# Optimization experiments

Hardware: AMD Instinct MI355X
Metric: run time of the kernel (lower is better)

## Reference

```python
import jax, jax.numpy as jnp
import numpy as np

NH, N = 48, 384
CARD, SUB, REPR, ENC = 16, 64, 1024, 1024
POOL_FEAT = 256 * 49


def _head_params(keys, app_size):
    k1, k2, k3 = keys
    W1 = jax.random.normal(k1, (CARD, app_size, SUB), jnp.float32) / np.sqrt(app_size)
    b1 = jnp.zeros((CARD, SUB), jnp.float32)
    W2 = jax.random.normal(k2, (CARD, REPR, SUB), jnp.float32) / np.sqrt(REPR)
    b2 = jnp.zeros((CARD, SUB), jnp.float32)
    W3 = jax.random.normal(k3, (CARD, SUB, REPR), jnp.float32) / np.sqrt(SUB)
    b3 = jnp.zeros((CARD, REPR), jnp.float32)
    return W1, b1, W2, b2, W3, b3


def setup_inputs() -> dict:
    key = jax.random.key(0)
    ks = list(jax.random.split(key, 24))
    d = {}
    d['box_features'] = jax.random.normal(ks[0], (N, POOL_FEAT), jnp.float32)
    d['feat3'] = jax.random.normal(ks[1], (1, 256, 25, 25), jnp.float32)
    d['spatial36'] = jax.random.uniform(ks[2], (NH * N, 36), jnp.float32)
    d['Wbh1'] = jax.random.normal(ks[3], (POOL_FEAT, ENC), jnp.float32) / np.sqrt(POOL_FEAT)
    d['bbh1'] = jnp.zeros(ENC, jnp.float32)
    d['Wbh2'] = jax.random.normal(ks[4], (ENC, ENC), jnp.float32) / np.sqrt(ENC)
    d['bbh2'] = jnp.zeros(ENC, jnp.float32)
    d['Wsp1'] = jax.random.normal(ks[5], (36, 128), jnp.float32) / 6.0
    d['bsp1'] = jnp.zeros(128, jnp.float32)
    d['Wsp2'] = jax.random.normal(ks[6], (128, 256), jnp.float32) / np.sqrt(128)
    d['bsp2'] = jnp.zeros(256, jnp.float32)
    d['Wsp3'] = jax.random.normal(ks[7], (256, REPR), jnp.float32) / 16.0
    d['bsp3'] = jnp.zeros(REPR, jnp.float32)
    d['Wadj'] = jax.random.normal(ks[8], (REPR, 1), jnp.float32) / 32.0
    d['badj'] = jnp.zeros(1, jnp.float32)
    for pre, app, k0 in (('A', 2 * ENC, 9), ('O', ENC, 12), ('S', ENC, 15), ('G', 256, 18)):
        W1, b1, W2, b2, W3, b3 = _head_params(ks[k0:k0 + 3], app)
        d[pre + '1W'], d[pre + '1b'] = W1, b1
        d[pre + '2W'], d[pre + '2b'] = W2, b2
        d[pre + '3W'], d[pre + '3b'] = W3, b3
    d['gln_h'] = jnp.ones(ENC, jnp.float32)
    d['bln_h'] = jnp.zeros(ENC, jnp.float32)
    d['gln_o'] = jnp.ones(ENC, jnp.float32)
    d['bln_o'] = jnp.zeros(ENC, jnp.float32)
    d['n_h'] = NH
    return d


def _attn_head(app, sp, W1, b1, W2, b2, W3, b3):
    # app [P_or_1, A], sp [P, REPR] -> relu(sum_c fc3_c(relu(fc1_c(app)*fc2_c(sp))))
    u = jnp.einsum('pa,cas->cps', app, W1) + b1[:, None, :]
    v = jnp.einsum('ps,csd->cpd', sp, W2) + b2[:, None, :]
    t = jax.nn.relu(u * v)  # broadcasts when app has leading 1
    return jax.nn.relu(jnp.einsum('cpd,cdr->pr', t, W3) + b3.sum(0))


def _msg_obj(app, sp, W1, b1, W2, b2, W3, b3):
    # app [n, ENC], sp [h, n, REPR] -> [h, n, REPR]  (object->subject messages)
    u = jnp.einsum('ne,ces->cns', app, W1) + b1[:, None, :]
    v = jnp.einsum('hns,csd->chnd', sp, W2) + b2[:, None, None, :]
    t = jax.nn.relu(u[:, None, :, :] * v)
    return jnp.einsum('chnd,cdr->hnr', t, W3) + b3.sum(0)


def _msg_hum(app, sp, W1, b1, W2, b2, W3, b3):
    # app [h, ENC], sp [h, n, REPR] -> [n, h, REPR]  (subject->object messages)
    u = jnp.einsum('he,ces->chs', app, W1) + b1[:, None, :]
    v = jnp.einsum('hns,csd->cnhd', sp, W2) + b2[:, None, None, :]
    t = jax.nn.relu(u[:, None, :, :] * v)
    return jnp.einsum('cnhd,cdr->nhr', t, W3) + b3.sum(0)


def _ln(x, g, b):
    mu = x.mean(-1, keepdims=True)
    var = jnp.mean((x - mu) ** 2, -1, keepdims=True)
    return (x - mu) * jax.lax.rsqrt(var + 1e-5) * g + b


def reference(box_features, feat3, spatial36, Wbh1, bbh1, Wbh2, bbh2,
              Wsp1, bsp1, Wsp2, bsp2, Wsp3, bsp3, Wadj, badj,
              A1W, A1b, A2W, A2b, A3W, A3b,
              O1W, O1b, O2W, O2b, O3W, O3b,
              S1W, S1b, S2W, S2b, S3W, S3b,
              G1W, G1b, G2W, G2b, G3W, G3b,
              gln_h, bln_h, gln_o, bln_o, n_h):
    h = int(n_h)
    n = box_features.shape[0]
    gfeat = feat3.mean(axis=(2, 3))  # [1, 256] (AdaptiveAvgPool2d(1) + flatten)
    # box_head MLP
    node = jax.nn.relu(box_features @ Wbh1 + bbh1)
    node = jax.nn.relu(node @ Wbh2 + bbh2)  # [n, ENC]
    # spatial_head MLP
    sp = jax.nn.relu(spatial36 @ Wsp1 + bsp1)
    sp = jax.nn.relu(sp @ Wsp2 + bsp2)
    sp = jax.nn.relu(sp @ Wsp3 + bsp3)  # [h*n, REPR]
    sp_r = sp.reshape(h, n, -1)
    x = np.repeat(np.arange(h), n)  # static pair indices
    y = np.tile(np.arange(n), h)
    h_node = node[:h]
    # one message-passing iteration (num_iter=1)
    pair_app = jnp.concatenate([h_node[x], node[y]], axis=1)  # [h*n, 2*ENC]
    w = _attn_head(pair_app, sp, A1W, A1b, A2W, A2b, A3W, A3b)
    adj = (w @ Wadj + badj).reshape(h, n)
    m_h = jax.nn.relu(jnp.sum(jax.nn.softmax(adj, axis=1)[..., None]
                              * _msg_obj(node, sp_r, O1W, O1b, O2W, O2b, O3W, O3b), axis=1))
    h_node = _ln(h_node + m_h, gln_h, bln_h)
    m_o = jax.nn.relu(jnp.sum(jax.nn.softmax(adj.T, axis=1)[..., None]
                              * _msg_hum(h_node, sp_r, S1W, S1b, S2W, S2b, S3W, S3b), axis=1))
    node = _ln(node + m_o, gln_o, bln_o)
    # static keep mask: drop pairs with identical indices (x != y)
    keep = x != y
    xk, yk = x[keep], y[keep]
    sp_k = sp_r[xk, yk]  # [Pk, REPR]
    f_pair = _attn_head(jnp.concatenate([h_node[xk], node[yk]], axis=1), sp_k,
                        A1W, A1b, A2W, A2b, A3W, A3b)
    f_glob = _attn_head(gfeat, sp_k, G1W, G1b, G2W, G2b, G3W, G3b)
    return jnp.concatenate([f_pair, f_glob], axis=1)  # [Pk, 2*REPR]
```

## Files before the change

kernel.cpp:

```cpp
#include <hip/hip_runtime.h>
#include <math.h>

#define NHH 48
#define NNN 384
#define NP  18432
#define NEC 1024

#define BM 128
#define BN 128
#define BK 32
#define KPAD 40

typedef __attribute__((ext_vector_type(8))) short short8v;
typedef __attribute__((ext_vector_type(4))) float f32x4;

__device__ __forceinline__ unsigned short f2bf(float x) {
  unsigned int u = __float_as_uint(x);
  u += 0x7fffu + ((u >> 16) & 1u);
  return (unsigned short)(u >> 16);
}
__device__ __forceinline__ float bf2f(unsigned short b) {
  return __uint_as_float(((unsigned)b) << 16);
}

__global__ __launch_bounds__(256) void convw_k(const float* __restrict__ in,
    unsigned short* __restrict__ out, int K, int N, int blocked)
{
  __shared__ float t[64][65];
  int kb = blockIdx.x * 64, nb = blockIdx.y * 64;
  const float* src; size_t stride;
  if (blocked) { src = in + (size_t)(nb >> 6) * K * 64; stride = 64; }
  else         { src = in + nb; stride = N; }
  for (int i = threadIdx.x; i < 64 * 64; i += 256) {
    int k = i >> 6, d = i & 63;
    t[d][k] = src[(size_t)(kb + k) * stride + d];
  }
  __syncthreads();
  for (int i = threadIdx.x; i < 64 * 64; i += 256) {
    int d = i >> 6, k = i & 63;
    out[(size_t)(nb + d) * K + kb + k] = f2bf(t[d][k]);
  }
}

__global__ __launch_bounds__(256) void cvt_k(const float* __restrict__ in,
    unsigned short* __restrict__ out, int n)
{
  int i = (blockIdx.x * 256 + threadIdx.x) * 4;
  if (i < n) {
    float4 v = *(const float4*)(in + i);
    uint2 o;
    o.x = (unsigned)f2bf(v.x) | ((unsigned)f2bf(v.y) << 16);
    o.y = (unsigned)f2bf(v.z) | ((unsigned)f2bf(v.w) << 16);
    *(uint2*)(out + i) = o;
  }
}

template<int MODE, int CBF16>
__global__ __launch_bounds__(256) void gemm_db(
    const unsigned short* __restrict__ A, const unsigned short* __restrict__ B,
    void* __restrict__ Cv, int M, int N, int K, int Ks,
    const float* __restrict__ bias, int do_relu,
    const float* __restrict__ x1, const float* __restrict__ x2,
    float* __restrict__ part, int colofs, int swz)
{
  __shared__ unsigned short As[2][BM * KPAD];
  __shared__ unsigned short Bs[2][BN * KPAD];
  __shared__ float red2[BM][2];

  const int tid  = threadIdx.x;
  const int lane = tid & 63;
  const int wave = tid >> 6;
  const int wr = wave >> 1, wc = wave & 1;
  const int lm = lane & 15;
  const int kg = lane >> 4;

  int bx = blockIdx.x, by = blockIdx.y;
  const int bz = blockIdx.z;
  if (swz) {
    int L = by * 8 + bx;
    int r = L & 7, q = L >> 3;
    bx = q & 7;
    by = r + ((q >> 3) << 3);
  }
  const int m0 = by * BM, n0 = bx * BN;
  const int kbeg = bz * Ks;
  const int kend = min(K, kbeg + Ks);
  const int nt = (kend - kbeg) / BK;

  f32x4 acc[4][4];
#pragma unroll
  for (int i = 0; i < 4; ++i)
#pragma unroll
    for (int j = 0; j < 4; ++j)
      acc[i][j] = (f32x4){0.f, 0.f, 0.f, 0.f};

  const int sr = tid >> 1;
  const int sc = (tid & 1) * 16;
  const unsigned short* aP = A + (size_t)(m0 + sr) * K + sc;
  const unsigned short* bP = B + (size_t)(n0 + sr) * K + sc;
  const int wofs = sr * KPAD + sc;

  uint4 ra0, ra1, rb0, rb1;
  uint4 sa0, sa1, sb0, sb1;

  auto fetchR = [&](int k0) {
    ra0 = *(const uint4*)(aP + k0); ra1 = *(const uint4*)(aP + k0 + 8);
    rb0 = *(const uint4*)(bP + k0); rb1 = *(const uint4*)(bP + k0 + 8);
  };
  auto fetchS = [&](int k0) {
    sa0 = *(const uint4*)(aP + k0); sa1 = *(const uint4*)(aP + k0 + 8);
    sb0 = *(const uint4*)(bP + k0); sb1 = *(const uint4*)(bP + k0 + 8);
  };
  auto writeR = [&](int buf) {
    *(uint4*)&As[buf][wofs] = ra0; *(uint4*)&As[buf][wofs + 8] = ra1;
    *(uint4*)&Bs[buf][wofs] = rb0; *(uint4*)&Bs[buf][wofs + 8] = rb1;
  };
  auto writeS = [&](int buf) {
    *(uint4*)&As[buf][wofs] = sa0; *(uint4*)&As[buf][wofs + 8] = sa1;
    *(uint4*)&Bs[buf][wofs] = sb0; *(uint4*)&Bs[buf][wofs + 8] = sb1;
  };
  auto computeBuf = [&](const unsigned short* as, const unsigned short* bs) {
    const int lk = kg * 8;
    short8v af[4], bfr[4];
#pragma unroll
    for (int mi = 0; mi < 4; ++mi)
      af[mi] = *(const short8v*)&as[(wr * 64 + mi * 16 + lm) * KPAD + lk];
#pragma unroll
    for (int nj = 0; nj < 4; ++nj)
      bfr[nj] = *(const short8v*)&bs[(wc * 64 + nj * 16 + lm) * KPAD + lk];
#pragma unroll
    for (int mi = 0; mi < 4; ++mi)
#pragma unroll
      for (int nj = 0; nj < 4; ++nj)
        acc[mi][nj] = __builtin_amdgcn_mfma_f32_16x16x32_bf16(af[mi], bfr[nj], acc[mi][nj], 0, 0, 0);
  };

  fetchR(kbeg);
  if (nt > 1) fetchS(kbeg + BK);
  writeR(0);
  if (nt > 2) fetchR(kbeg + 2 * BK);
  __syncthreads();

  for (int it = 0; it < nt; it += 2) {
    writeS(1);
    if (it + 3 < nt) fetchS(kbeg + (it + 3) * BK);
    computeBuf(&As[0][0], &Bs[0][0]);
    __syncthreads();
    if (it + 2 < nt) writeR(0);
    if (it + 4 < nt) fetchR(kbeg + (it + 4) * BK);
    computeBuf(&As[1][0], &Bs[1][0]);
    __syncthreads();
  }

  const int rbase = m0 + wr * 64;
  const int cbase = n0 + wc * 64;

  if constexpr (MODE == 0 || MODE == 3) {
#pragma unroll
    for (int mi = 0; mi < 4; ++mi)
#pragma unroll
      for (int r = 0; r < 4; ++r) {
        int grow = rbase + mi * 16 + kg * 4 + r;
#pragma unroll
        for (int nj = 0; nj < 4; ++nj) {
          int gcol = cbase + nj * 16 + lm;
          float t = acc[mi][nj][r] + (bias ? bias[gcol] : 0.f);
          float v;
          if constexpr (MODE == 3) v = fmaxf(x1[gcol] * t, 0.f);
          else                     v = do_relu ? fmaxf(t, 0.f) : t;
          size_t idx = (size_t)grow * N + gcol;
          if constexpr (CBF16) ((unsigned short*)Cv)[idx] = f2bf(v);
          else                 ((float*)Cv)[idx] = v;
        }
      }
  } else if constexpr (MODE == 5) {
    size_t zofs = (size_t)bz * M;
#pragma unroll
    for (int mi = 0; mi < 4; ++mi)
#pragma unroll
      for (int r = 0; r < 4; ++r) {
        int grow = rbase + mi * 16 + kg * 4 + r;
#pragma unroll
        for (int nj = 0; nj < 4; ++nj) {
          int gcol = cbase + nj * 16 + lm;
          part[(zofs + grow) * N + gcol] = acc[mi][nj][r];
        }
      }
  } else if constexpr (MODE == 2) {
#pragma unroll
    for (int mi = 0; mi < 4; ++mi)
#pragma unroll
      for (int r = 0; r < 4; ++r) {
        int grow = rbase + mi * 16 + kg * 4 + r;
        int h = grow / NNN, n = grow - h * NNN;
        if (n == h) continue;
        long long orow = grow - h - (n > h ? 1 : 0);
#pragma unroll
        for (int nj = 0; nj < 4; ++nj) {
          int gcol = cbase + nj * 16 + lm;
          float v = fmaxf(acc[mi][nj][r] + bias[gcol], 0.f);
          ((float*)Cv)[orow * 2048 + colofs + gcol] = v;
        }
      }
  } else if constexpr (MODE == 1) {
#pragma unroll
    for (int mi = 0; mi < 4; ++mi)
#pragma unroll
      for (int r = 0; r < 4; ++r) {
        float s = 0.f;
#pragma unroll
        for (int nj = 0; nj < 4; ++nj) {
          int gcol = cbase + nj * 16 + lm;
          float v = fmaxf(acc[mi][nj][r] + bias[gcol], 0.f);
          s = fmaf(v, x1[gcol], s);
        }
#pragma unroll
        for (int off2 = 1; off2 < 16; off2 <<= 1) s += __shfl_xor(s, off2);
        if (lm == 0) red2[wr * 64 + mi * 16 + kg * 4 + r][wc] = s;
      }
    __syncthreads();
    if (tid < BM) {
      part[(size_t)(m0 + tid) * 8 + bx] = red2[tid][0] + red2[tid][1];
    }
  }
}

__global__ __launch_bounds__(256) void tmulb_k(const unsigned short* __restrict__ vA,
    const float* __restrict__ uh, const float* __restrict__ un,
    unsigned short* __restrict__ V)
{
  int p = blockIdx.x;
  int h = p / NNN, n = p - h * NNN;
  int j = threadIdx.x * 4;
  const float* uhr = uh + (size_t)h * NEC + j;
  const float* unr = un + (size_t)n * NEC + j;
  uint2 w = *(const uint2*)(vA + (size_t)p * NEC + j);
  float v0 = bf2f((unsigned short)(w.x & 0xffff));
  float v1 = bf2f((unsigned short)(w.x >> 16));
  float v2 = bf2f((unsigned short)(w.y & 0xffff));
  float v3 = bf2f((unsigned short)(w.y >> 16));
  float f0 = fmaxf((uhr[0] + unr[0]) * v0, 0.f);
  float f1 = fmaxf((uhr[1] + unr[1]) * v1, 0.f);
  float f2 = fmaxf((uhr[2] + unr[2]) * v2, 0.f);
  float f3 = fmaxf((uhr[3] + unr[3]) * v3, 0.f);
  uint2 o;
  o.x = (unsigned)f2bf(f0) | ((unsigned)f2bf(f1) << 16);
  o.y = (unsigned)f2bf(f2) | ((unsigned)f2bf(f3) << 16);
  *(uint2*)(V + (size_t)p * NEC + j) = o;
}

template<int MODE, int ABF16, int BBF16, int CBF16>
__global__ __launch_bounds__(256) void gemm_mfma(
    const void* __restrict__ Av, const void* __restrict__ Bv, long long ldbBlock,
    void* __restrict__ Cv, int M, int N, int K, int Ks,
    const float* __restrict__ bias, int do_relu,
    const float* __restrict__ x1, const float* __restrict__ x2,
    float* __restrict__ part, int colofs, int swz)
{
  __shared__ unsigned short As[BM * KPAD];
  __shared__ unsigned short Bs[BN * KPAD];

  const float* Af = (const float*)Av;
  const unsigned short* Ab = (const unsigned short*)Av;
  const float* Bf = (const float*)Bv;
  const unsigned short* Bb = (const unsigned short*)Bv;

  const int tid  = threadIdx.x;
  const int lane = tid & 63;
  const int wave = tid >> 6;
  const int wr = wave >> 1, wc = wave & 1;
  const int lm = lane & 15;
  const int kg = lane >> 4;

  int bx = blockIdx.x, by = blockIdx.y, bz = blockIdx.z;
  if (swz == 2) {
    int gy = gridDim.y;
    int ntile = gy * gridDim.z;
    int L = (bz * gy + by) * 8 + bx;
    int r = L & 7, q = L >> 3;
    int tpx = ntile >> 3;
    int tile = r * tpx + (q >> 3);
    bx = q & 7;
    bz = tile / gy;
    by = tile - bz * gy;
  }
  const int m0 = by * BM, n0 = bx * BN;
  const int kbeg = bz * Ks;
  const int kend = min(K, kbeg + Ks);

  f32x4 acc[4][4];
#pragma unroll
  for (int i = 0; i < 4; ++i)
#pragma unroll
    for (int j = 0; j < 4; ++j)
      acc[i][j] = (f32x4){0.f, 0.f, 0.f, 0.f};

  const int bn = tid & 127;
  const int kb = (tid >> 7) * 16;
  const float* bsrc = nullptr; long long bstride = 0;
  if constexpr (!BBF16) {
    int gcol = n0 + bn;
    if (ldbBlock) { bsrc = Bf + (long long)(gcol >> 6) * ldbBlock + (gcol & 63); bstride = 64; }
    else          { bsrc = Bf + gcol; bstride = N; }
  }

  uint4 pa0 = {0,0,0,0}, pa1 = {0,0,0,0};
  uint2 qa0 = {0,0}, qa1 = {0,0}, qa2 = {0,0}, qa3 = {0,0};
  uint4 pb0 = {0,0,0,0}, pb1 = {0,0,0,0};

  auto fetchA = [&](int k0) {
    if constexpr (ABF16) {
      int m = tid >> 1, kh = (tid & 1) * 16;
      int gm = m0 + m;
      pa0 = (uint4){0,0,0,0}; pa1 = (uint4){0,0,0,0};
      if (gm < M) {
        const uint4* s = (const uint4*)(Ab + (size_t)gm * K + k0 + kh);
        pa0 = s[0]; pa1 = s[1];
      }
    } else {
#define LOADA_F32(J, DST) { \
      int m = (tid >> 3) + J * 32; int k = (tid & 7) * 4; \
      int gm = m0 + m, gk = k0 + k; \
      float x0=0.f, x1v=0.f, x2v=0.f, x3=0.f; \
      if (gm < M) { const float* src = Af + (long long)gm * K + gk; \
        if (gk + 3 < K) { float4 v = *(const float4*)src; x0=v.x; x1v=v.y; x2v=v.z; x3=v.w; } \
        else { if (gk < K) x0 = src[0]; if (gk+1 < K) x1v = src[1]; \
               if (gk+2 < K) x2v = src[2]; if (gk+3 < K) x3 = src[3]; } } \
      DST.x = (unsigned)f2bf(x0)  | ((unsigned)f2bf(x1v) << 16); \
      DST.y = (unsigned)f2bf(x2v) | ((unsigned)f2bf(x3)  << 16); }
      LOADA_F32(0, qa0) LOADA_F32(1, qa1) LOADA_F32(2, qa2) LOADA_F32(3, qa3)
#undef LOADA_F32
    }
  };
  auto fetchB = [&](int k0) {
    if constexpr (BBF16) {
      int nrow = tid >> 1, kh = (tid & 1) * 16;
      const uint4* s = (const uint4*)(Bb + (size_t)(n0 + nrow) * K + k0 + kh);
      pb0 = s[0]; pb1 = s[1];
    } else {
#define PACKB(I, DST) { int g0 = k0 + kb + 2*I, g1 = g0 + 1; \
      float a = (g0 < K) ? bsrc[(long long)g0 * bstride] : 0.f; \
      float c = (g1 < K) ? bsrc[(long long)g1 * bstride] : 0.f; \
      DST = (unsigned)f2bf(a) | ((unsigned)f2bf(c) << 16); }
      PACKB(0, pb0.x) PACKB(1, pb0.y) PACKB(2, pb0.z) PACKB(3, pb0.w)
      PACKB(4, pb1.x) PACKB(5, pb1.y) PACKB(6, pb1.z) PACKB(7, pb1.w)
#undef PACKB
    }
  };
  auto stage = [&]() {
    if constexpr (ABF16) {
      int m = tid >> 1, kh = (tid & 1) * 16;
      *(uint4*)&As[m * KPAD + kh]     = pa0;
      *(uint4*)&As[m * KPAD + kh + 8] = pa1;
    } else {
      int m = tid >> 3, k = (tid & 7) * 4;
      *(uint2*)&As[(m      ) * KPAD + k] = qa0;
      *(uint2*)&As[(m +  32) * KPAD + k] = qa1;
      *(uint2*)&As[(m +  64) * KPAD + k] = qa2;
      *(uint2*)&As[(m +  96) * KPAD + k] = qa3;
    }
    if constexpr (BBF16) {
      int nrow = tid >> 1, kh = (tid & 1) * 16;
      *(uint4*)&Bs[nrow * KPAD + kh]     = pb0;
      *(uint4*)&Bs[nrow * KPAD + kh + 8] = pb1;
    } else {
      *(uint4*)&Bs[bn * KPAD + kb]     = pb0;
      *(uint4*)&Bs[bn * KPAD + kb + 8] = pb1;
    }
  };

  fetchA(kbeg); fetchB(kbeg);
  for (int k0 = kbeg; k0 < kend; k0 += BK) {
    stage();
    int kn = k0 + BK;
    if (kn < kend) { fetchA(kn); fetchB(kn); }
    __syncthreads();
    {
      const int lk = kg * 8;
      short8v af[4], bfr[4];
#pragma unroll
      for (int mi = 0; mi < 4; ++mi)
        af[mi] = *(const short8v*)&As[(wr * 64 + mi * 16 + lm) * KPAD + lk];
#pragma unroll
      for (int nj = 0; nj < 4; ++nj)
        bfr[nj] = *(const short8v*)&Bs[(wc * 64 + nj * 16 + lm) * KPAD + lk];
#pragma unroll
      for (int mi = 0; mi < 4; ++mi)
#pragma unroll
        for (int nj = 0; nj < 4; ++nj)
          acc[mi][nj] = __builtin_amdgcn_mfma_f32_16x16x32_bf16(af[mi], bfr[nj], acc[mi][nj], 0, 0, 0);
    }
    __syncthreads();
  }

  const int rbase = m0 + wr * 64;
  const int cbase = n0 + wc * 64;

  if constexpr (MODE == 0) {
#pragma unroll
    for (int mi = 0; mi < 4; ++mi)
#pragma unroll
      for (int r = 0; r < 4; ++r) {
        int grow = rbase + mi * 16 + kg * 4 + r;
        if (grow >= M) continue;
#pragma unroll
        for (int nj = 0; nj < 4; ++nj) {
          int gcol = cbase + nj * 16 + lm;
          float t = acc[mi][nj][r] + (bias ? bias[gcol] : 0.f);
          float v = do_relu ? fmaxf(t, 0.f) : t;
          size_t idx = (size_t)grow * N + gcol;
          if constexpr (CBF16) ((unsigned short*)Cv)[idx] = f2bf(v);
          else                 ((float*)Cv)[idx] = v;
        }
      }
  } else if constexpr (MODE == 5) {
    size_t zofs = (size_t)bz * M;
#pragma unroll
    for (int mi = 0; mi < 4; ++mi)
#pragma unroll
      for (int r = 0; r < 4; ++r) {
        int grow = rbase + mi * 16 + kg * 4 + r;
        if (grow >= M) continue;
#pragma unroll
        for (int nj = 0; nj < 4; ++nj) {
          int gcol = cbase + nj * 16 + lm;
          part[(zofs + grow) * N + gcol] = acc[mi][nj][r];
        }
      }
  }
}

__global__ __launch_bounds__(256) void ksum_k(const float* __restrict__ P,
    const float* __restrict__ bias, int do_relu, float* __restrict__ C,
    int MN, int N, int S)
{
  int i = blockIdx.x * 256 + threadIdx.x;
  if (i < MN) {
    float s = 0.f;
    for (int z = 0; z < S; ++z) s += P[(size_t)z * MN + i];
    if (bias) s += bias[i % N];
    C[i] = do_relu ? fmaxf(s, 0.f) : s;
  }
}

__global__ __launch_bounds__(256) void tw_k(const unsigned short* __restrict__ V,
    const float* __restrict__ uO, const float* __restrict__ soft, float* __restrict__ tw)
{
  int h = blockIdx.x;
  int j = blockIdx.y * 256 + threadIdx.x;
  const float* srow = soft + h * NNN;
  float s = 0.f;
  for (int n = 0; n < NNN; ++n) {
    float v = bf2f(V[((size_t)h * NNN + n) * NEC + j]);
    float t = fmaxf(uO[(size_t)n * NEC + j] * v, 0.f);
    s = fmaf(srow[n], t, s);
  }
  tw[(size_t)h * NEC + j] = s;
}

__global__ __launch_bounds__(256) void two_k(const unsigned short* __restrict__ V,
    const float* __restrict__ uS, const float* __restrict__ softT, float* __restrict__ two)
{
  int n = blockIdx.x;
  int j = blockIdx.y * 256 + threadIdx.x;
  const float* srow = softT + n * NHH;
  float s = 0.f;
#pragma unroll 8
  for (int h = 0; h < NHH; ++h) {
    float v = bf2f(V[((size_t)h * NNN + n) * NEC + j]);
    float t = fmaxf(uS[(size_t)h * NEC + j] * v, 0.f);
    s = fmaf(srow[h], t, s);
  }
  two[(size_t)n * NEC + j] = s;
}

__global__ void adjfin_k(const float* __restrict__ part, const float* __restrict__ badj,
                         float* __restrict__ adj)
{
  int p = blockIdx.x * blockDim.x + threadIdx.x;
  if (p < NP) {
    float s = badj[0];
#pragma unroll
    for (int c = 0; c < 8; ++c) s += part[(size_t)p * 8 + c];
    adj[p] = s;
  }
}

__global__ __launch_bounds__(64) void softmax_row_k(const float* __restrict__ adj,
                                                    float* __restrict__ soft)
{
  __shared__ float buf[NNN];
  int h = blockIdx.x, t = threadIdx.x;
  float mx = -1e30f;
  for (int n = t; n < NNN; n += 64) { float v = adj[h * NNN + n]; buf[n] = v; mx = fmaxf(mx, v); }
#pragma unroll
  for (int off = 32; off >= 1; off >>= 1) mx = fmaxf(mx, __shfl_xor(mx, off));
  float s = 0.f;
  for (int n = t; n < NNN; n += 64) { float e = expf(buf[n] - mx); buf[n] = e; s += e; }
#pragma unroll
  for (int off = 32; off >= 1; off >>= 1) s += __shfl_xor(s, off);
  float inv = 1.f / s;
  for (int n = t; n < NNN; n += 64) soft[h * NNN + n] = buf[n] * inv;
}

__global__ __launch_bounds__(64) void softmaxT_k(const float* __restrict__ adj,
                                                 float* __restrict__ softT)
{
  int n = blockIdx.x, t = threadIdx.x;
  float v = (t < NHH) ? adj[t * NNN + n] : -1e30f;
  float mx = v;
#pragma unroll
  for (int off = 32; off >= 1; off >>= 1) mx = fmaxf(mx, __shfl_xor(mx, off));
  float e = (t < NHH) ? expf(v - mx) : 0.f;
  float s = e;
#pragma unroll
  for (int off = 32; off >= 1; off >>= 1) s += __shfl_xor(s, off);
  if (t < NHH) softT[n * NHH + t] = e / s;
}

__global__ __launch_bounds__(256) void ln_k(const float* __restrict__ x, const float* __restrict__ m,
    const float* __restrict__ g, const float* __restrict__ b, float* __restrict__ out)
{
  int r = blockIdx.x, t = threadIdx.x;
  __shared__ float rs[4], rs2[4];
  const float* xr = x + (size_t)r * NEC;
  const float* mr = m + (size_t)r * NEC;
  float s = 0.f, s2 = 0.f;
  for (int j = t; j < NEC; j += 256) { float v = xr[j] + mr[j]; s += v; s2 = fmaf(v, v, s2); }
#pragma unroll
  for (int off = 32; off >= 1; off >>= 1) { s += __shfl_xor(s, off); s2 += __shfl_xor(s2, off); }
  if ((t & 63) == 0) { rs[t >> 6] = s; rs2[t >> 6] = s2; }
  __syncthreads();
  s = rs[0] + rs[1] + rs[2] + rs[3];
  s2 = rs2[0] + rs2[1] + rs2[2] + rs2[3];
  float mean = s * (1.f / NEC);
  float var = s2 * (1.f / NEC) - mean * mean;
  float rstd = rsqrtf(var + 1e-5f);
  float* o = out + (size_t)r * NEC;
  for (int j = t; j < NEC; j += 256) {
    float v = xr[j] + mr[j];
    o[j] = (v - mean) * rstd * g[j] + b[j];
  }
}

__global__ __launch_bounds__(64) void gfeat_k(const float* __restrict__ feat3,
                                              float* __restrict__ gfeat)
{
  int ch = blockIdx.x, t = threadIdx.x;
  float s = 0.f;
  for (int i = t; i < 625; i += 64) s += feat3[ch * 625 + i];
#pragma unroll
  for (int off = 32; off >= 1; off >>= 1) s += __shfl_xor(s, off);
  if (t == 0) gfeat[ch] = s * (1.f / 625.f);
}

__global__ __launch_bounds__(256) void b3sum_k(const float* __restrict__ b3,
                                               float* __restrict__ out)
{
  int r = blockIdx.x * 256 + threadIdx.x;
  if (r < NEC) {
    float s = 0.f;
#pragma unroll
    for (int c = 0; c < 16; ++c) s += b3[c * NEC + r];
    out[r] = s;
  }
}

extern "C" void kernel_launch(void* const* d_in, const int* in_sizes, int n_in,
                              void* d_out, int out_size, void* d_ws, size_t ws_size,
                              hipStream_t stream)
{
  const float* box   = (const float*)d_in[0];
  const float* feat3 = (const float*)d_in[1];
  const float* sp36  = (const float*)d_in[2];
  const float* Wbh1  = (const float*)d_in[3];
  const float* bbh1  = (const float*)d_in[4];
  const float* Wbh2  = (const float*)d_in[5];
  const float* bbh2  = (const float*)d_in[6];
  const float* Wsp1  = (const float*)d_in[7];
  const float* bsp1  = (const float*)d_in[8];
  const float* Wsp2  = (const float*)d_in[9];
  const float* bsp2  = (const float*)d_in[10];
  const float* Wsp3  = (const float*)d_in[11];
  const float* bsp3  = (const float*)d_in[12];
  const float* Wadj  = (const float*)d_in[13];
  const float* badj  = (const float*)d_in[14];
  const float* A1W = (const float*)d_in[15]; const float* A1b = (const float*)d_in[16];
  const float* A2W = (const float*)d_in[17]; const float* A2b = (const float*)d_in[18];
  const float* A3W = (const float*)d_in[19]; const float* A3b = (const float*)d_in[20];
  const float* O1W = (const float*)d_in[21]; const float* O1b = (const float*)d_in[22];
  const float* O2W = (const float*)d_in[23]; const float* O2b = (const float*)d_in[24];
  const float* O3W = (const float*)d_in[25]; const float* O3b = (const float*)d_in[26];
  const float* S1W = (const float*)d_in[27]; const float* S1b = (const float*)d_in[28];
  const float* S2W = (const float*)d_in[29]; const float* S2b = (const float*)d_in[30];
  const float* S3W = (const float*)d_in[31]; const float* S3b = (const float*)d_in[32];
  const float* G1W = (const float*)d_in[33]; const float* G1b = (const float*)d_in[34];
  const float* G2W = (const float*)d_in[35]; const float* G2b = (const float*)d_in[36];
  const float* G3W = (const float*)d_in[37]; const float* G3b = (const float*)d_in[38];
  const float* gln_h = (const float*)d_in[39]; const float* bln_h = (const float*)d_in[40];
  const float* gln_o = (const float*)d_in[41]; const float* bln_o = (const float*)d_in[42];
  (void)in_sizes; (void)n_in; (void)out_size; (void)ws_size;

  char* base = (char*)d_ws;
  unsigned short* Vb  = (unsigned short*)base;
  float* partial      = (float*)base;
  unsigned short* s1  = Vb;
  unsigned short* s2  = Vb + (size_t)NP * 128;
  unsigned short* SPb = (unsigned short*)(base + (size_t)NP * NEC * 2);
  float* f = (float*)(base + (size_t)NP * NEC * 4);
  size_t off = 0;
  auto alloc = [&](size_t n) { float* p = f + off; off += n; return p; };
  float* node1 = alloc(384 * NEC);
  float* node  = alloc(384 * NEC);
  float* hnode1= alloc(48 * NEC);
  float* node2 = alloc(384 * NEC);
  float* uhA   = alloc(48 * NEC);
  float* unA   = alloc(384 * NEC);
  float* uO    = alloc(384 * NEC);
  float* uS    = alloc(48 * NEC);
  float* uh2   = alloc(48 * NEC);
  float* un2   = alloc(384 * NEC);
  float* uG    = alloc(NEC);
  float* gfeat = alloc(256);
  float* b3A = alloc(NEC); float* b3O = alloc(NEC); float* b3S = alloc(NEC); float* b3G = alloc(NEC);
  float* part  = alloc((size_t)NP * 8);
  float* adj   = alloc(NP);
  float* soft  = alloc(NP);
  float* softT = alloc(NP);
  float* twb   = alloc(48 * NEC);
  float* twob  = alloc(384 * NEC);
  float* m_h   = alloc(48 * NEC);
  float* m_o   = alloc(384 * NEC);
  unsigned short* wb = (unsigned short*)(f + off);
  size_t wo = 0;
  auto walloc = [&](size_t n) { unsigned short* p = wb + wo; wo += n; return p; };
  unsigned short* A2Wb  = walloc((size_t)NEC * NEC);
  unsigned short* O2Wb  = walloc((size_t)NEC * NEC);
  unsigned short* S2Wb  = walloc((size_t)NEC * NEC);
  unsigned short* G2Wb  = walloc((size_t)NEC * NEC);
  unsigned short* A3Wb  = walloc((size_t)NEC * NEC);
  unsigned short* G3Wb  = walloc((size_t)NEC * NEC);
  unsigned short* Wsp3b = walloc((size_t)NEC * 256);
  unsigned short* Wsp2b = walloc((size_t)256 * 128);
  unsigned short* vAb   = walloc((size_t)NP * NEC);
  unsigned short* Wbh1b = walloc((size_t)NEC * 12544);
  unsigned short* boxb  = walloc((size_t)384 * 12544);

  auto gS = [&](const float* A, const float* B, long long lb, float* C,
                int M, int N, int K, const float* bias, int relu, int S) {
    int Ks = ((K + S * BK - 1) / (S * BK)) * BK;
    dim3 grid(N / BN, (M + BM - 1) / BM, S);
    hipLaunchKernelGGL((gemm_mfma<5, 0, 0, 0>), grid, dim3(256), 0, stream,
                       A, B, lb, nullptr, M, N, K, Ks, nullptr, 0,
                       nullptr, nullptr, partial, 0, 2);
    int MN = M * N;
    hipLaunchKernelGGL(ksum_k, dim3((MN + 255) / 256), dim3(256), 0, stream,
                       partial, bias, relu, C, MN, N, S);
  };
  auto convw = [&](const float* W, unsigned short* Wb2, int K, int N, int blocked) {
    dim3 g(K / 64, N / 64);
    hipLaunchKernelGGL(convw_k, g, dim3(256), 0, stream, W, Wb2, K, N, blocked);
  };

  convw(A2W, A2Wb, NEC, NEC, 1);
  convw(O2W, O2Wb, NEC, NEC, 1);
  convw(S2W, S2Wb, NEC, NEC, 1);
  convw(G2W, G2Wb, NEC, NEC, 1);
  convw(A3W, A3Wb, NEC, NEC, 0);
  convw(G3W, G3Wb, NEC, NEC, 0);
  convw(Wsp3, Wsp3b, 256, NEC, 0);
  convw(Wsp2, Wsp2b, 128, 256, 0);
  convw(Wbh1, Wbh1b, 12544, NEC, 0);
  cvt_k<<<(384 * 12544 / 4 + 255) / 256, 256, 0, stream>>>(box, boxb, 384 * 12544);

  gfeat_k<<<256, 64, 0, stream>>>(feat3, gfeat);
  b3sum_k<<<4, 256, 0, stream>>>(A3b, b3A);
  b3sum_k<<<4, 256, 0, stream>>>(O3b, b3O);
  b3sum_k<<<4, 256, 0, stream>>>(S3b, b3S);
  b3sum_k<<<4, 256, 0, stream>>>(G3b, b3G);

  {
    dim3 grid(NEC / BN, 384 / BM, 28);
    hipLaunchKernelGGL((gemm_db<5, 0>), grid, dim3(256), 0, stream,
                       boxb, Wbh1b, nullptr, 384, NEC, 12544, 448, nullptr, 0,
                       nullptr, nullptr, partial, 0, 0);
    int MN = 384 * NEC;
    hipLaunchKernelGGL(ksum_k, dim3((MN + 255) / 256), dim3(256), 0, stream,
                       partial, bbh1, 1, node1, MN, NEC, 28);
  }
  gS(node1, Wbh2, 0, node, 384, NEC, NEC, bbh2, 1, 16);

  dim3 gBig(8, NP / BM);

  {
    dim3 g1(1, NP / BM); dim3 g2(2, NP / BM);
    hipLaunchKernelGGL((gemm_mfma<0, 0, 0, 1>), g1, dim3(256), 0, stream,
                       sp36, Wsp1, 0LL, s1, NP, 128, 36, 36, bsp1, 1, nullptr, nullptr, nullptr, 0, 0);
    hipLaunchKernelGGL((gemm_db<0, 1>), g2, dim3(256), 0, stream,
                       s1, Wsp2b, s2, NP, 256, 128, 128, bsp2, 1, nullptr, nullptr, nullptr, 0, 0);
    hipLaunchKernelGGL((gemm_db<0, 1>), gBig, dim3(256), 0, stream,
                       s2, Wsp3b, SPb, NP, NEC, 256, 256, bsp3, 1, nullptr, nullptr, nullptr, 0, 1);
  }

  hipLaunchKernelGGL((gemm_db<0, 1>), gBig, dim3(256), 0, stream,
                     SPb, A2Wb, vAb, NP, NEC, NEC, NEC, A2b, 0, nullptr, nullptr, nullptr, 0, 1);

  gS(node, A1W,             2048LL * 64, uhA, 48,  NEC, NEC, A1b,    0, 16);
  gS(node, A1W + 1024 * 64, 2048LL * 64, unA, 384, NEC, NEC, nullptr, 0, 16);
  tmulb_k<<<NP, 256, 0, stream>>>(vAb, uhA, unA, Vb);
  hipLaunchKernelGGL((gemm_db<1, 0>), gBig, dim3(256), 0, stream,
                     Vb, A3Wb, nullptr, NP, NEC, NEC, NEC, b3A, 1, Wadj, nullptr, part, 0, 1);
  adjfin_k<<<(NP + 255) / 256, 256, 0, stream>>>(part, badj, adj);
  softmax_row_k<<<NHH, 64, 0, stream>>>(adj, soft);
  softmaxT_k<<<NNN, 64, 0, stream>>>(adj, softT);

  gS(node, O1W, 1024LL * 64, uO, 384, NEC, NEC, O1b, 0, 16);
  hipLaunchKernelGGL((gemm_db<0, 1>), gBig, dim3(256), 0, stream,
                     SPb, O2Wb, Vb, NP, NEC, NEC, NEC, O2b, 0, nullptr, nullptr, nullptr, 0, 1);
  tw_k<<<dim3(NHH, 4), 256, 0, stream>>>(Vb, uO, soft, twb);
  gS(twb, O3W, 0, m_h, 48, NEC, NEC, b3O, 1, 16);
  ln_k<<<NHH, 256, 0, stream>>>(node, m_h, gln_h, bln_h, hnode1);

  gS(hnode1, S1W, 1024LL * 64, uS, 48, NEC, NEC, S1b, 0, 16);
  hipLaunchKernelGGL((gemm_db<0, 1>), gBig, dim3(256), 0, stream,
                     SPb, S2Wb, Vb, NP, NEC, NEC, NEC, S2b, 0, nullptr, nullptr, nullptr, 0, 1);
  two_k<<<dim3(NNN, 4), 256, 0, stream>>>(Vb, uS, softT, twob);
  gS(twob, S3W, 0, m_o, 384, NEC, NEC, b3S, 1, 16);
  ln_k<<<NNN, 256, 0, stream>>>(node, m_o, gln_o, bln_o, node2);

  gS(hnode1, A1W,             2048LL * 64, uh2, 48,  NEC, NEC, A1b,    0, 16);
  gS(node2,  A1W + 1024 * 64, 2048LL * 64, un2, 384, NEC, NEC, nullptr, 0, 16);
  tmulb_k<<<NP, 256, 0, stream>>>(vAb, uh2, un2, Vb);
  hipLaunchKernelGGL((gemm_db<2, 0>), gBig, dim3(256), 0, stream,
                     Vb, A3Wb, (float*)d_out, NP, NEC, NEC, NEC, b3A, 1, nullptr, nullptr, nullptr, 0, 1);

  {
    dim3 g1(8, 1);
    hipLaunchKernelGGL((gemm_mfma<0, 0, 0, 0>), g1, dim3(256), 0, stream,
                       gfeat, G1W, 256LL * 64, uG, 1, NEC, 256, 256, G1b, 0, nullptr, nullptr, nullptr, 0, 0);
  }
  hipLaunchKernelGGL((gemm_db<3, 1>), gBig, dim3(256), 0, stream,
                     SPb, G2Wb, Vb, NP, NEC, NEC, NEC, G2b, 0, uG, nullptr, nullptr, 0, 1);
  hipLaunchKernelGGL((gemm_db<2, 0>), gBig, dim3(256), 0, stream,
                     Vb, G3Wb, (float*)d_out, NP, NEC, NEC, NEC, b3G, 1, nullptr, nullptr, nullptr, 1024, 1);
}
```

Measured before the change: 870.5 us.

## Batch the four spatial fc2 GEMMs into one wide GEMM and group node projections

The four separate SP×W2 GEMMs (A, O, S, G heads) become one NP×4096 GEMM that reads SP once. Its epilogue applies the per-column bias and, for the G slice, the uG gating. The small node-side projections (uhA/unA/uO, uS/uh2) are grouped into wider bf16 split-K GEMMs with a grouped reduction kernel, and the fp32 mfma GEMMs are replaced with bf16 gemm_db. This removes repeated reads of SP and several launches. The cost is a larger workspace holding the 4096-wide V buffer and strided accesses in the downstream consumers.

```diff
diff --git a/kernel.cpp b/kernel.cpp
--- a/kernel.cpp
+++ b/kernel.cpp
@@ -5,6 +5,7 @@
 #define NNN 384
 #define NP  18432
 #define NEC 1024
+#define MB1 (1024*1024)
 
 #define BM 128
 #define BN 128
@@ -24,21 +25,21 @@
 }
 
 __global__ __launch_bounds__(256) void convw_k(const float* __restrict__ in,
-    unsigned short* __restrict__ out, int K, int N, int blocked)
+    unsigned short* __restrict__ out, int inK, int outK, int N, int blocked, int koff)
 {
   __shared__ float t[64][65];
   int kb = blockIdx.x * 64, nb = blockIdx.y * 64;
   const float* src; size_t stride;
-  if (blocked) { src = in + (size_t)(nb >> 6) * K * 64; stride = 64; }
+  if (blocked) { src = in + (size_t)(nb >> 6) * inK * 64; stride = 64; }
   else         { src = in + nb; stride = N; }
   for (int i = threadIdx.x; i < 64 * 64; i += 256) {
     int k = i >> 6, d = i & 63;
-    t[d][k] = src[(size_t)(kb + k) * stride + d];
+    t[d][k] = src[(size_t)(kb + koff + k) * stride + d];
   }
   __syncthreads();
   for (int i = threadIdx.x; i < 64 * 64; i += 256) {
     int d = i >> 6, k = i & 63;
-    out[(size_t)(nb + d) * K + kb + k] = f2bf(t[d][k]);
+    out[(size_t)(nb + d) * outK + kb + k] = f2bf(t[d][k]);
   }
 }
 
@@ -55,9 +56,22 @@
   }
 }
 
+__global__ __launch_bounds__(256) void biascat4_k(const float* __restrict__ b0,
+    const float* __restrict__ b1, const float* __restrict__ b2,
+    const float* __restrict__ b3, float* __restrict__ out)
+{
+  int j = blockIdx.x * 256 + threadIdx.x;
+  if (j < 4096) {
+    int g = j >> 10, c = j & 1023;
+    const float* b = g == 0 ? b0 : (g == 1 ? b1 : (g == 2 ? b2 : b3));
+    out[j] = b[c];
+  }
+}
+
 template<int MODE, int CBF16>
 __global__ __launch_bounds__(256) void gemm_db(
-    const unsigned short* __restrict__ A, const unsigned short* __restrict__ B,
+    const unsigned short* __restrict__ A, int lda,
+    const unsigned short* __restrict__ B, int ldb,
     void* __restrict__ Cv, int M, int N, int K, int Ks,
     const float* __restrict__ bias, int do_relu,
     const float* __restrict__ x1, const float* __restrict__ x2,
@@ -77,10 +91,11 @@
   int bx = blockIdx.x, by = blockIdx.y;
   const int bz = blockIdx.z;
   if (swz) {
-    int L = by * 8 + bx;
+    int gx = gridDim.x;
+    int L = by * gx + bx;
     int r = L & 7, q = L >> 3;
-    bx = q & 7;
-    by = r + ((q >> 3) << 3);
+    bx = q % gx;
+    by = r + 8 * (q / gx);
   }
   const int m0 = by * BM, n0 = bx * BN;
   const int kbeg = bz * Ks;
@@ -96,8 +111,8 @@
 
   const int sr = tid >> 1;
   const int sc = (tid & 1) * 16;
-  const unsigned short* aP = A + (size_t)(m0 + sr) * K + sc;
-  const unsigned short* bP = B + (size_t)(n0 + sr) * K + sc;
+  const unsigned short* aP = A + (size_t)(m0 + sr) * lda + sc;
+  const unsigned short* bP = B + (size_t)(n0 + sr) * ldb + sc;
   const int wofs = sr * KPAD + sc;
 
   uint4 ra0, ra1, rb0, rb1;
@@ -155,7 +170,7 @@
   const int rbase = m0 + wr * 64;
   const int cbase = n0 + wc * 64;
 
-  if constexpr (MODE == 0 || MODE == 3) {
+  if constexpr (MODE == 0) {
 #pragma unroll
     for (int mi = 0; mi < 4; ++mi)
 #pragma unroll
@@ -165,12 +180,24 @@
         for (int nj = 0; nj < 4; ++nj) {
           int gcol = cbase + nj * 16 + lm;
           float t = acc[mi][nj][r] + (bias ? bias[gcol] : 0.f);
-          float v;
-          if constexpr (MODE == 3) v = fmaxf(x1[gcol] * t, 0.f);
-          else                     v = do_relu ? fmaxf(t, 0.f) : t;
+          float v = do_relu ? fmaxf(t, 0.f) : t;
           size_t idx = (size_t)grow * N + gcol;
           if constexpr (CBF16) ((unsigned short*)Cv)[idx] = f2bf(v);
           else                 ((float*)Cv)[idx] = v;
+        }
+      }
+  } else if constexpr (MODE == 6) {
+#pragma unroll
+    for (int mi = 0; mi < 4; ++mi)
+#pragma unroll
+      for (int r = 0; r < 4; ++r) {
+        int grow = rbase + mi * 16 + kg * 4 + r;
+#pragma unroll
+        for (int nj = 0; nj < 4; ++nj) {
+          int gcol = cbase + nj * 16 + lm;
+          float t = acc[mi][nj][r] + bias[gcol];
+          float v = (gcol >= 3072) ? fmaxf(x1[gcol - 3072] * t, 0.f) : t;
+          ((unsigned short*)Cv)[(size_t)grow * N + gcol] = f2bf(v);
         }
       }
   } else if constexpr (MODE == 5) {
@@ -226,7 +253,7 @@
 }
 
 __global__ __launch_bounds__(256) void tmulb_k(const unsigned short* __restrict__ vA,
-    const float* __restrict__ uh, const float* __restrict__ un,
+    int vstride, const float* __restrict__ uh, const float* __restrict__ un,
     unsigned short* __restrict__ V)
 {
   int p = blockIdx.x;
@@ -234,7 +261,7 @@
   int j = threadIdx.x * 4;
   const float* uhr = uh + (size_t)h * NEC + j;
   const float* unr = un + (size_t)n * NEC + j;
-  uint2 w = *(const uint2*)(vA + (size_t)p * NEC + j);
+  uint2 w = *(const uint2*)(vA + (size_t)p * vstride + j);
   float v0 = bf2f((unsigned short)(w.x & 0xffff));
   float v1 = bf2f((unsigned short)(w.x >> 16));
   float v2 = bf2f((unsigned short)(w.y & 0xffff));
@@ -443,7 +470,27 @@
   }
 }
 
-__global__ __launch_bounds__(256) void tw_k(const unsigned short* __restrict__ V,
+__global__ __launch_bounds__(256) void ksumg_k(const float* __restrict__ P,
+    const float* __restrict__ b0, const float* __restrict__ b1, const float* __restrict__ b2,
+    float* __restrict__ C0, float* __restrict__ C1, float* __restrict__ C2,
+    int M, int NG, int S)
+{
+  int i = blockIdx.x * 256 + threadIdx.x;
+  int N = NG << 10;
+  int total = M * N;
+  if (i < total) {
+    int m = i / N, c = i - m * N;
+    int g = c >> 10, col = c & 1023;
+    float s = 0.f;
+    for (int z = 0; z < S; ++z) s += P[(size_t)z * total + i];
+    const float* b = g == 0 ? b0 : (g == 1 ? b1 : b2);
+    if (b) s += b[col];
+    float* C = g == 0 ? C0 : (g == 1 ? C1 : C2);
+    C[(size_t)m * 1024 + col] = s;
+  }
+}
+
+__global__ __launch_bounds__(256) void tw_k(const unsigned short* __restrict__ V, int sV,
     const float* __restrict__ uO, const float* __restrict__ soft, float* __restrict__ tw)
 {
   int h = blockIdx.x;
@@ -451,14 +498,14 @@
   const float* srow = soft + h * NNN;
   float s = 0.f;
   for (int n = 0; n < NNN; ++n) {
-    float v = bf2f(V[((size_t)h * NNN + n) * NEC + j]);
+    float v = bf2f(V[((size_t)h * NNN + n) * sV + j]);
     float t = fmaxf(uO[(size_t)n * NEC + j] * v, 0.f);
     s = fmaf(srow[n], t, s);
   }
   tw[(size_t)h * NEC + j] = s;
 }
 
-__global__ __launch_bounds__(256) void two_k(const unsigned short* __restrict__ V,
+__global__ __launch_bounds__(256) void two_k(const unsigned short* __restrict__ V, int sV,
     const float* __restrict__ uS, const float* __restrict__ softT, float* __restrict__ two)
 {
   int n = blockIdx.x;
@@ -467,7 +514,7 @@
   float s = 0.f;
 #pragma unroll 8
   for (int h = 0; h < NHH; ++h) {
-    float v = bf2f(V[((size_t)h * NNN + n) * NEC + j]);
+    float v = bf2f(V[((size_t)h * NNN + n) * sV + j]);
     float t = fmaxf(uS[(size_t)h * NEC + j] * v, 0.f);
     s = fmaf(srow[h], t, s);
   }
@@ -602,27 +649,30 @@
   (void)in_sizes; (void)n_in; (void)out_size; (void)ws_size;
 
   char* base = (char*)d_ws;
-  unsigned short* Vb  = (unsigned short*)base;
-  float* partial      = (float*)base;
+  unsigned short* V4  = (unsigned short*)base;
+  float* partialV4    = (float*)base;
+  unsigned short* Vb  = (unsigned short*)(base + (size_t)NP * 4096 * 2);
+  float* partialVb    = (float*)Vb;
   unsigned short* s1  = Vb;
   unsigned short* s2  = Vb + (size_t)NP * 128;
-  unsigned short* SPb = (unsigned short*)(base + (size_t)NP * NEC * 2);
-  float* f = (float*)(base + (size_t)NP * NEC * 4);
+  unsigned short* SPb = Vb + (size_t)NP * 1024;
+  float* f = (float*)(SPb + (size_t)NP * 1024);
   size_t off = 0;
   auto alloc = [&](size_t n) { float* p = f + off; off += n; return p; };
   float* node1 = alloc(384 * NEC);
   float* node  = alloc(384 * NEC);
-  float* hnode1= alloc(48 * NEC);
+  float* hnode1= alloc(128 * NEC);
   float* node2 = alloc(384 * NEC);
-  float* uhA   = alloc(48 * NEC);
+  float* uhA   = alloc(384 * NEC);
   float* unA   = alloc(384 * NEC);
   float* uO    = alloc(384 * NEC);
-  float* uS    = alloc(48 * NEC);
-  float* uh2   = alloc(48 * NEC);
+  float* uS    = alloc(128 * NEC);
+  float* uh2   = alloc(128 * NEC);
   float* un2   = alloc(384 * NEC);
   float* uG    = alloc(NEC);
   float* gfeat = alloc(256);
   float* b3A = alloc(NEC); float* b3O = alloc(NEC); float* b3S = alloc(NEC); float* b3G = alloc(NEC);
+  float* bias4 = alloc(4096);
   float* part  = alloc((size_t)NP * 8);
   float* adj   = alloc(NP);
   float* soft  = alloc(NP);
@@ -634,43 +684,53 @@
   unsigned short* wb = (unsigned short*)(f + off);
   size_t wo = 0;
   auto walloc = [&](size_t n) { unsigned short* p = wb + wo; wo += n; return p; };
-  unsigned short* A2Wb  = walloc((size_t)NEC * NEC);
-  unsigned short* O2Wb  = walloc((size_t)NEC * NEC);
-  unsigned short* S2Wb  = walloc((size_t)NEC * NEC);
-  unsigned short* G2Wb  = walloc((size_t)NEC * NEC);
-  unsigned short* A3Wb  = walloc((size_t)NEC * NEC);
-  unsigned short* G3Wb  = walloc((size_t)NEC * NEC);
+  unsigned short* W4b   = walloc((size_t)4 * MB1);
+  unsigned short* A3Wb  = walloc((size_t)MB1);
+  unsigned short* G3Wb  = walloc((size_t)MB1);
   unsigned short* Wsp3b = walloc((size_t)NEC * 256);
   unsigned short* Wsp2b = walloc((size_t)256 * 128);
-  unsigned short* vAb   = walloc((size_t)NP * NEC);
   unsigned short* Wbh1b = walloc((size_t)NEC * 12544);
+  unsigned short* Wbh2b = walloc((size_t)MB1);
+  unsigned short* U1b   = walloc((size_t)3 * MB1);
+  unsigned short* U2b   = walloc((size_t)2 * MB1);
   unsigned short* boxb  = walloc((size_t)384 * 12544);
-
+  unsigned short* nodeb = walloc((size_t)384 * NEC);
+  unsigned short* node1b= walloc((size_t)384 * NEC);
+  unsigned short* hnode1b = walloc((size_t)128 * NEC);
+  unsigned short* node2b  = walloc((size_t)384 * NEC);
+
+  auto convw = [&](const float* W, unsigned short* out, int inK, int outK, int N,
+                   int blocked, int koff) {
+    dim3 g(outK / 64, N / 64);
+    hipLaunchKernelGGL(convw_k, g, dim3(256), 0, stream, W, out, inK, outK, N, blocked, koff);
+  };
   auto gS = [&](const float* A, const float* B, long long lb, float* C,
                 int M, int N, int K, const float* bias, int relu, int S) {
     int Ks = ((K + S * BK - 1) / (S * BK)) * BK;
     dim3 grid(N / BN, (M + BM - 1) / BM, S);
     hipLaunchKernelGGL((gemm_mfma<5, 0, 0, 0>), grid, dim3(256), 0, stream,
                        A, B, lb, nullptr, M, N, K, Ks, nullptr, 0,
-                       nullptr, nullptr, partial, 0, 2);
+                       nullptr, nullptr, partialVb, 0, 2);
     int MN = M * N;
     hipLaunchKernelGGL(ksum_k, dim3((MN + 255) / 256), dim3(256), 0, stream,
-                       partial, bias, relu, C, MN, N, S);
-  };
-  auto convw = [&](const float* W, unsigned short* Wb2, int K, int N, int blocked) {
-    dim3 g(K / 64, N / 64);
-    hipLaunchKernelGGL(convw_k, g, dim3(256), 0, stream, W, Wb2, K, N, blocked);
-  };
-
-  convw(A2W, A2Wb, NEC, NEC, 1);
-  convw(O2W, O2Wb, NEC, NEC, 1);
-  convw(S2W, S2Wb, NEC, NEC, 1);
-  convw(G2W, G2Wb, NEC, NEC, 1);
-  convw(A3W, A3Wb, NEC, NEC, 0);
-  convw(G3W, G3Wb, NEC, NEC, 0);
-  convw(Wsp3, Wsp3b, 256, NEC, 0);
-  convw(Wsp2, Wsp2b, 128, 256, 0);
-  convw(Wbh1, Wbh1b, 12544, NEC, 0);
+                       partialVb, bias, relu, C, MN, N, S);
+  };
+
+  convw(A2W, W4b + 0 * MB1, NEC, NEC, NEC, 1, 0);
+  convw(O2W, W4b + 1 * MB1, NEC, NEC, NEC, 1, 0);
+  convw(S2W, W4b + 2 * MB1, NEC, NEC, NEC, 1, 0);
+  convw(G2W, W4b + 3 * MB1, NEC, NEC, NEC, 1, 0);
+  convw(A3W, A3Wb, NEC, NEC, NEC, 0, 0);
+  convw(G3W, G3Wb, NEC, NEC, NEC, 0, 0);
+  convw(Wsp3, Wsp3b, 256, 256, NEC, 0, 0);
+  convw(Wsp2, Wsp2b, 128, 128, 256, 0, 0);
+  convw(Wbh1, Wbh1b, 12544, 12544, NEC, 0, 0);
+  convw(Wbh2, Wbh2b, NEC, NEC, NEC, 0, 0);
+  convw(A1W, U1b + 0 * MB1, 2048, NEC, NEC, 1, 0);
+  convw(A1W, U1b + 1 * MB1, 2048, NEC, NEC, 1, 1024);
+  convw(O1W, U1b + 2 * MB1, NEC, NEC, NEC, 1, 0);
+  convw(S1W, U2b + 0 * MB1, NEC, NEC, NEC, 1, 0);
+  convw(A1W, U2b + 1 * MB1, 2048, NEC, NEC, 1, 0);
   cvt_k<<<(384 * 12544 / 4 + 255) / 256, 256, 0, stream>>>(box, boxb, 384 * 12544);
 
   gfeat_k<<<256, 64, 0, stream>>>(feat3, gfeat);
@@ -678,69 +738,117 @@
   b3sum_k<<<4, 256, 0, stream>>>(O3b, b3O);
   b3sum_k<<<4, 256, 0, stream>>>(S3b, b3S);
   b3sum_k<<<4, 256, 0, stream>>>(G3b, b3G);
-
-  {
-    dim3 grid(NEC / BN, 384 / BM, 28);
+  biascat4_k<<<16, 256, 0, stream>>>(A2b, O2b, S2b, G2b, bias4);
+
+  {
+    dim3 grid(8, 3, 28);
     hipLaunchKernelGGL((gemm_db<5, 0>), grid, dim3(256), 0, stream,
-                       boxb, Wbh1b, nullptr, 384, NEC, 12544, 448, nullptr, 0,
-                       nullptr, nullptr, partial, 0, 0);
-    int MN = 384 * NEC;
-    hipLaunchKernelGGL(ksum_k, dim3((MN + 255) / 256), dim3(256), 0, stream,
-                       partial, bbh1, 1, node1, MN, NEC, 28);
-  }
-  gS(node1, Wbh2, 0, node, 384, NEC, NEC, bbh2, 1, 16);
-
-  dim3 gBig(8, NP / BM);
-
-  {
-    dim3 g1(1, NP / BM); dim3 g2(2, NP / BM);
+                       boxb, 12544, Wbh1b, 12544, nullptr, 384, NEC, 12544, 448,
+                       nullptr, 0, nullptr, nullptr, partialV4, 0, 0);
+    hipLaunchKernelGGL(ksum_k, dim3((384 * NEC + 255) / 256), dim3(256), 0, stream,
+                       partialV4, bbh1, 1, node1, 384 * NEC, NEC, 28);
+  }
+  cvt_k<<<(384 * NEC / 4 + 255) / 256, 256, 0, stream>>>(node1, node1b, 384 * NEC);
+  {
+    dim3 grid(8, 3, 8);
+    hipLaunchKernelGGL((gemm_db<5, 0>), grid, dim3(256), 0, stream,
+                       node1b, NEC, Wbh2b, NEC, nullptr, 384, NEC, NEC, 128,
+                       nullptr, 0, nullptr, nullptr, partialV4, 0, 0);
+    hipLaunchKernelGGL(ksum_k, dim3((384 * NEC + 255) / 256), dim3(256), 0, stream,
+                       partialV4, bbh2, 1, node, 384 * NEC, NEC, 8);
+  }
+  cvt_k<<<(384 * NEC / 4 + 255) / 256, 256, 0, stream>>>(node, nodeb, 384 * NEC);
+
+  {
+    dim3 g1(1, NP / BM);
     hipLaunchKernelGGL((gemm_mfma<0, 0, 0, 1>), g1, dim3(256), 0, stream,
                        sp36, Wsp1, 0LL, s1, NP, 128, 36, 36, bsp1, 1, nullptr, nullptr, nullptr, 0, 0);
+    dim3 g2(2, NP / BM);
     hipLaunchKernelGGL((gemm_db<0, 1>), g2, dim3(256), 0, stream,
-                       s1, Wsp2b, s2, NP, 256, 128, 128, bsp2, 1, nullptr, nullptr, nullptr, 0, 0);
-    hipLaunchKernelGGL((gemm_db<0, 1>), gBig, dim3(256), 0, stream,
-                       s2, Wsp3b, SPb, NP, NEC, 256, 256, bsp3, 1, nullptr, nullptr, nullptr, 0, 1);
-  }
-
-  hipLaunchKernelGGL((gemm_db<0, 1>), gBig, dim3(256), 0, stream,
-                     SPb, A2Wb, vAb, NP, NEC, NEC, NEC, A2b, 0, nullptr, nullptr, nullptr, 0, 1);
-
-  gS(node, A1W,             2048LL * 64, uhA, 48,  NEC, NEC, A1b,    0, 16);
-  gS(node, A1W + 1024 * 64, 2048LL * 64, unA, 384, NEC, NEC, nullptr, 0, 16);
-  tmulb_k<<<NP, 256, 0, stream>>>(vAb, uhA, unA, Vb);
-  hipLaunchKernelGGL((gemm_db<1, 0>), gBig, dim3(256), 0, stream,
-                     Vb, A3Wb, nullptr, NP, NEC, NEC, NEC, b3A, 1, Wadj, nullptr, part, 0, 1);
+                       s1, 128, Wsp2b, 128, s2, NP, 256, 128, 128, bsp2, 1,
+                       nullptr, nullptr, nullptr, 0, 0);
+    dim3 g3(8, NP / BM);
+    hipLaunchKernelGGL((gemm_db<0, 1>), g3, dim3(256), 0, stream,
+                       s2, 256, Wsp3b, 256, SPb, NP, NEC, 256, 256, bsp3, 1,
+                       nullptr, nullptr, nullptr, 0, 1);
+  }
+
+  {
+    dim3 g1(8, 1);
+    hipLaunchKernelGGL((gemm_mfma<0, 0, 0, 0>), g1, dim3(256), 0, stream,
+                       gfeat, G1W, 256LL * 64, uG, 1, NEC, 256, 256, G1b, 0,
+                       nullptr, nullptr, nullptr, 0, 0);
+  }
+
+  {
+    dim3 grid(32, NP / BM);
+    hipLaunchKernelGGL((gemm_db<6, 1>), grid, dim3(256), 0, stream,
+                       SPb, NEC, W4b, NEC, V4, NP, 4096, NEC, NEC,
+                       bias4, 0, uG, nullptr, nullptr, 0, 1);
+  }
+
+  {
+    dim3 grid(24, 3, 8);
+    hipLaunchKernelGGL((gemm_db<5, 0>), grid, dim3(256), 0, stream,
+                       nodeb, NEC, U1b, NEC, nullptr, 384, 3072, NEC, 128,
+                       nullptr, 0, nullptr, nullptr, partialVb, 0, 0);
+    int total = 384 * 3072;
+    hipLaunchKernelGGL(ksumg_k, dim3((total + 255) / 256), dim3(256), 0, stream,
+                       partialVb, A1b, (const float*)nullptr, O1b, uhA, unA, uO, 384, 3, 8);
+  }
+
+  tmulb_k<<<NP, 256, 0, stream>>>(V4 + 0, 4096, uhA, unA, Vb);
+  {
+    dim3 g(8, NP / BM);
+    hipLaunchKernelGGL((gemm_db<1, 0>), g, dim3(256), 0, stream,
+                       Vb, NEC, A3Wb, NEC, nullptr, NP, NEC, NEC, NEC,
+                       b3A, 1, Wadj, nullptr, part, 0, 1);
+  }
   adjfin_k<<<(NP + 255) / 256, 256, 0, stream>>>(part, badj, adj);
   softmax_row_k<<<NHH, 64, 0, stream>>>(adj, soft);
   softmaxT_k<<<NNN, 64, 0, stream>>>(adj, softT);
 
-  gS(node, O1W, 1024LL * 64, uO, 384, NEC, NEC, O1b, 0, 16);
-  hipLaunchKernelGGL((gemm_db<0, 1>), gBig, dim3(256), 0, stream,
-                     SPb, O2Wb, Vb, NP, NEC, NEC, NEC, O2b, 0, nullptr, nullptr, nullptr, 0, 1);
-  tw_k<<<dim3(NHH, 4), 256, 0, stream>>>(Vb, uO, soft, twb);
+  tw_k<<<dim3(NHH, 4), 256, 0, stream>>>(V4 + 1024, 4096, uO, soft, twb);
   gS(twb, O3W, 0, m_h, 48, NEC, NEC, b3O, 1, 16);
   ln_k<<<NHH, 256, 0, stream>>>(node, m_h, gln_h, bln_h, hnode1);
-
-  gS(hnode1, S1W, 1024LL * 64, uS, 48, NEC, NEC, S1b, 0, 16);
-  hipLaunchKernelGGL((gemm_db<0, 1>), gBig, dim3(256), 0, stream,
-                     SPb, S2Wb, Vb, NP, NEC, NEC, NEC, S2b, 0, nullptr, nullptr, nullptr, 0, 1);
-  two_k<<<dim3(NNN, 4), 256, 0, stream>>>(Vb, uS, softT, twob);
+  cvt_k<<<(128 * NEC / 4 + 255) / 256, 256, 0, stream>>>(hnode1, hnode1b, 128 * NEC);
+
+  {
+    dim3 grid(16, 1, 8);
+    hipLaunchKernelGGL((gemm_db<5, 0>), grid, dim3(256), 0, stream,
+                       hnode1b, NEC, U2b, NEC, nullptr, 128, 2048, NEC, 128,
+                       nullptr, 0, nullptr, nullptr, partialVb, 0, 0);
+    int total = 128 * 2048;
+    hipLaunchKernelGGL(ksumg_k, dim3((total + 255) / 256), dim3(256), 0, stream,
+                       partialVb, S1b, A1b, (const float*)nullptr, uS, uh2, (float*)nullptr, 128, 2, 8);
+  }
+
+  two_k<<<dim3(NNN, 4), 256, 0, stream>>>(V4 + 2048, 4096, uS, softT, twob);
   gS(twob, S3W, 0, m_o, 384, NEC, NEC, b3S, 1, 16);
   ln_k<<<NNN, 256, 0, stream>>>(node, m_o, gln_o, bln_o, node2);
-
-  gS(hnode1, A1W,             2048LL * 64, uh2, 48,  NEC, NEC, A1b,    0, 16);
-  gS(node2,  A1W + 1024 * 64, 2048LL * 64, un2, 384, NEC, NEC, nullptr, 0, 16);
-  tmulb_k<<<NP, 256, 0, stream>>>(vAb, uh2, un2, Vb);
-  hipLaunchKernelGGL((gemm_db<2, 0>), gBig, dim3(256), 0, stream,
-                     Vb, A3Wb, (float*)d_out, NP, NEC, NEC, NEC, b3A, 1, nullptr, nullptr, nullptr, 0, 1);
-
-  {
-    dim3 g1(8, 1);
-    hipLaunchKernelGGL((gemm_mfma<0, 0, 0, 0>), g1, dim3(256), 0, stream,
-                       gfeat, G1W, 256LL * 64, uG, 1, NEC, 256, 256, G1b, 0, nullptr, nullptr, nullptr, 0, 0);
-  }
-  hipLaunchKernelGGL((gemm_db<3, 1>), gBig, dim3(256), 0, stream,
-                     SPb, G2Wb, Vb, NP, NEC, NEC, NEC, G2b, 0, uG, nullptr, nullptr, 0, 1);
-  hipLaunchKernelGGL((gemm_db<2, 0>), gBig, dim3(256), 0, stream,
-                     Vb, G3Wb, (float*)d_out, NP, NEC, NEC, NEC, b3G, 1, nullptr, nullptr, nullptr, 1024, 1);
-}
+  cvt_k<<<(384 * NEC / 4 + 255) / 256, 256, 0, stream>>>(node2, node2b, 384 * NEC);
+
+  {
+    dim3 grid(8, 3, 8);
+    hipLaunchKernelGGL((gemm_db<5, 0>), grid, dim3(256), 0, stream,
+                       node2b, NEC, U1b + 1 * MB1, NEC, nullptr, 384, NEC, NEC, 128,
+                       nullptr, 0, nullptr, nullptr, partialVb, 0, 0);
+    hipLaunchKernelGGL(ksum_k, dim3((384 * NEC + 255) / 256), dim3(256), 0, stream,
+                       partialVb, (const float*)nullptr, 0, un2, 384 * NEC, NEC, 8);
+  }
+
+  tmulb_k<<<NP, 256, 0, stream>>>(V4 + 0, 4096, uh2, un2, Vb);
+  {
+    dim3 g(8, NP / BM);
+    hipLaunchKernelGGL((gemm_db<2, 0>), g, dim3(256), 0, stream,
+                       Vb, NEC, A3Wb, NEC, (float*)d_out, NP, NEC, NEC, NEC,
+                       b3A, 1, nullptr, nullptr, nullptr, 0, 1);
+  }
+
+  {
+    dim3 g(8, NP / BM);
+    hipLaunchKernelGGL((gemm_db<2, 0>), g, dim3(256), 0, stream,
+                       V4 + 3072, 4096, G3Wb, NEC, (float*)d_out, NP, NEC, NEC, NEC,
+                       b3G, 1, nullptr, nullptr, nullptr, 1024, 1);
+  }
+}
```

New measurement: 868.8 us. No clear change (-0.2%).
